# Kernel tuning notes

Hardware: AMD Instinct MI355X
Metric: run time of the kernel (lower is better)

The kernel has to match this reference:

```python
import jax, jax.numpy as jnp
import numpy as np

COMMITMENT_COST = 0.25
EMBEDDING_COST = 1.0


def setup_inputs() -> dict:
    key = jax.random.key(0)
    k1, k2 = jax.random.split(key)
    x = jax.random.normal(k1, (64, 1024, 64), dtype=jnp.float32)
    embeddings = jax.random.normal(k2, (1024, 64), dtype=jnp.float32)
    return {"x": x, "embeddings": embeddings}


def reference(x, embeddings):
    D = embeddings.shape[1]
    flat_x = x.reshape(-1, D)  # [N, D]
    distances = (
        jnp.sum(flat_x ** 2, axis=1, keepdims=True)
        + jnp.sum(embeddings ** 2, axis=1)
        - 2.0 * flat_x @ embeddings.T
    )
    encoding_indices = jnp.argmin(distances, axis=1)  # [N]
    quantized = embeddings[encoding_indices].reshape(x.shape)
    q_latent_loss = jnp.mean((quantized - jax.lax.stop_gradient(x)) ** 2) * EMBEDDING_COST
    e_latent_loss = jnp.mean((x - jax.lax.stop_gradient(quantized)) ** 2) * COMMITMENT_COST
    loss = q_latent_loss + e_latent_loss
    # Straight-through estimator
    quantized_st = x + jax.lax.stop_gradient(quantized - x)
    return (quantized_st, loss)
```

## Files before the change

kernel.cpp:

```cpp
#include <hip/hip_runtime.h>
#include <math.h>

#define NROWS 65536
#define D 64
#define K 1024
#define BR 64
#define EC 128
#define NCH (K / EC)
#define THREADS 256
#define TAU 0.02f
#define LOSS_SCALE (1.25f / (65536.0f * 64.0f))

typedef short bf16x8 __attribute__((ext_vector_type(8)));
typedef float f32x4 __attribute__((ext_vector_type(4)));

__device__ inline unsigned short f2bf(float f) {
    unsigned int u = __float_as_uint(f);
    unsigned int r = u + 0x7fffu + ((u >> 16) & 1u);
    return (unsigned short)(r >> 16);
}
__device__ inline float bf2f(unsigned short h) {
    return __uint_as_float(((unsigned int)h) << 16);
}
__device__ inline void cvt8(const float4& a, const float4& b, bf16x8& h, bf16x8& l) {
    float f[8] = {a.x, a.y, a.z, a.w, b.x, b.y, b.z, b.w};
#pragma unroll
    for (int j = 0; j < 8; ++j) {
        unsigned short hb = f2bf(f[j]);
        h[j] = (short)hb;
        l[j] = (short)f2bf(f[j] - bf2f(hb));
    }
}

__global__ void vq_prep(const float* __restrict__ E, float* __restrict__ C,
                        bf16x8* __restrict__ Eh8, bf16x8* __restrict__ El8,
                        float* __restrict__ lossp, int* __restrict__ fcnt) {
    int k = blockIdx.x * blockDim.x + threadIdx.x;
    if (k == 0) { *lossp = 0.f; *fcnt = 0; }
    if (k >= K) return;
    const float4* ev = (const float4*)(E + (size_t)k * D);
    float s = 0.f;
#pragma unroll
    for (int u = 0; u < 8; ++u) {
        float4 a = ev[2 * u], b = ev[2 * u + 1];
        s = fmaf(a.x, a.x, s); s = fmaf(a.y, a.y, s);
        s = fmaf(a.z, a.z, s); s = fmaf(a.w, a.w, s);
        s = fmaf(b.x, b.x, s); s = fmaf(b.y, b.y, s);
        s = fmaf(b.z, b.z, s); s = fmaf(b.w, b.w, s);
        bf16x8 h, l;
        cvt8(a, b, h, l);
        Eh8[(size_t)k * 8 + u] = h;
        El8[(size_t)k * 8 + u] = l;
    }
    C[k] = s;
}

__global__ __launch_bounds__(THREADS, 4) void vq_main(
    const float* __restrict__ X, const float* __restrict__ E,
    const float* __restrict__ C,
    const bf16x8* __restrict__ Eh8, const bf16x8* __restrict__ El8,
    int* __restrict__ bestk, int* __restrict__ flags, int* __restrict__ fcnt,
    float* __restrict__ out, float* __restrict__ lossp)
{
    __shared__ bf16x8 sEh8[EC * 8];
    __shared__ bf16x8 sEl8[EC * 8];
    __shared__ float  sCn[EC];
    __shared__ int    sIdx[BR];
    __shared__ float  sLoss[4];

    const int t    = threadIdx.x;
    const int w    = t >> 6;
    const int lane = t & 63;
    const int l15  = lane & 15;
    const int l4   = lane >> 4;

    const float4* Xg4 = (const float4*)X;

    size_t abase = ((size_t)blockIdx.x * BR + w * 16 + l15) * 16;
    bf16x8 ah[2], al[2];
    float nrm = 0.f;
#pragma unroll
    for (int kt = 0; kt < 2; ++kt) {
        float4 fa = Xg4[abase + kt * 8 + l4 * 2];
        float4 fb = Xg4[abase + kt * 8 + l4 * 2 + 1];
        nrm = fmaf(fa.x, fa.x, nrm); nrm = fmaf(fa.y, fa.y, nrm);
        nrm = fmaf(fa.z, fa.z, nrm); nrm = fmaf(fa.w, fa.w, nrm);
        nrm = fmaf(fb.x, fb.x, nrm); nrm = fmaf(fb.y, fb.y, nrm);
        nrm = fmaf(fb.z, fb.z, nrm); nrm = fmaf(fb.w, fb.w, nrm);
        cvt8(fa, fb, ah[kt], al[kt]);
    }
    nrm += __shfl_xor(nrm, 16, 64);
    nrm += __shfl_xor(nrm, 32, 64);
    float rxv[4];
#pragma unroll
    for (int r = 0; r < 4; ++r) rxv[r] = __shfl(nrm, l4 * 4 + r, 64);

    float m[4], m2[4]; int bk[4];
#pragma unroll
    for (int r = 0; r < 4; ++r) { m[r] = INFINITY; m2[r] = INFINITY; bk[r] = 0; }

    for (int ch = 0; ch < NCH; ++ch) {
        __syncthreads();
#pragma unroll
        for (int p = 0; p < 4; ++p) {
            int S = p * 256 + t;
            int code = S >> 3, u8 = S & 7;
            int di = code * 8 + (u8 ^ (code & 7));
            sEh8[di] = Eh8[(size_t)ch * (EC * 8) + S];
            sEl8[di] = El8[(size_t)ch * (EC * 8) + S];
        }
        if (t < EC) sCn[t] = C[ch * EC + t];
        __syncthreads();

#pragma unroll 2
        for (int pr = 0; pr < 4; ++pr) {
            int c0 = pr * 32 + l15;
            int c1 = c0 + 16;
            int s0 = c0 & 7, s1 = c1 & 7;
            bf16x8 bh00 = sEh8[c0 * 8 + (l4 ^ s0)];
            bf16x8 bh01 = sEh8[c0 * 8 + ((4 + l4) ^ s0)];
            bf16x8 bl00 = sEl8[c0 * 8 + (l4 ^ s0)];
            bf16x8 bl01 = sEl8[c0 * 8 + ((4 + l4) ^ s0)];
            bf16x8 bh10 = sEh8[c1 * 8 + (l4 ^ s1)];
            bf16x8 bh11 = sEh8[c1 * 8 + ((4 + l4) ^ s1)];
            bf16x8 bl10 = sEl8[c1 * 8 + (l4 ^ s1)];
            bf16x8 bl11 = sEl8[c1 * 8 + ((4 + l4) ^ s1)];

            f32x4 h0 = {0.f, 0.f, 0.f, 0.f}, x0 = {0.f, 0.f, 0.f, 0.f};
            f32x4 h1 = {0.f, 0.f, 0.f, 0.f}, x1 = {0.f, 0.f, 0.f, 0.f};
            h0 = __builtin_amdgcn_mfma_f32_16x16x32_bf16(ah[0], bh00, h0, 0, 0, 0);
            h1 = __builtin_amdgcn_mfma_f32_16x16x32_bf16(ah[0], bh10, h1, 0, 0, 0);
            x0 = __builtin_amdgcn_mfma_f32_16x16x32_bf16(al[0], bh00, x0, 0, 0, 0);
            x1 = __builtin_amdgcn_mfma_f32_16x16x32_bf16(al[0], bh10, x1, 0, 0, 0);
            h0 = __builtin_amdgcn_mfma_f32_16x16x32_bf16(ah[1], bh01, h0, 0, 0, 0);
            h1 = __builtin_amdgcn_mfma_f32_16x16x32_bf16(ah[1], bh11, h1, 0, 0, 0);
            x0 = __builtin_amdgcn_mfma_f32_16x16x32_bf16(ah[0], bl00, x0, 0, 0, 0);
            x1 = __builtin_amdgcn_mfma_f32_16x16x32_bf16(ah[0], bl10, x1, 0, 0, 0);
            x0 = __builtin_amdgcn_mfma_f32_16x16x32_bf16(al[1], bh01, x0, 0, 0, 0);
            x1 = __builtin_amdgcn_mfma_f32_16x16x32_bf16(al[1], bh11, x1, 0, 0, 0);
            x0 = __builtin_amdgcn_mfma_f32_16x16x32_bf16(ah[1], bl01, x0, 0, 0, 0);
            x1 = __builtin_amdgcn_mfma_f32_16x16x32_bf16(ah[1], bl11, x1, 0, 0, 0);

            float ce0 = sCn[pr * 32 + l15];
            float ce1 = sCn[pr * 32 + 16 + l15];
            int k0 = ch * EC + pr * 32 + l15;
            int k1 = k0 + 16;
#pragma unroll
            for (int r = 0; r < 4; ++r) {
                float d0 = fmaf(-2.f, h0[r] + x0[r], rxv[r] + ce0);
                m2[r] = fminf(m2[r], fmaxf(m[r], d0));
                bk[r] = (d0 < m[r]) ? k0 : bk[r];
                m[r]  = fminf(m[r], d0);
                float d1 = fmaf(-2.f, h1[r] + x1[r], rxv[r] + ce1);
                m2[r] = fminf(m2[r], fmaxf(m[r], d1));
                bk[r] = (d1 < m[r]) ? k1 : bk[r];
                m[r]  = fminf(m[r], d1);
            }
        }
    }

#pragma unroll
    for (int r = 0; r < 4; ++r) {
        float mm = m[r], mm2 = m2[r]; int kk = bk[r];
#pragma unroll
        for (int off = 1; off < 16; off <<= 1) {
            float om  = __shfl_xor(mm,  off, 64);
            float om2 = __shfl_xor(mm2, off, 64);
            int   ok  = __shfl_xor(kk,  off, 64);
            mm2 = fminf(fminf(mm2, om2), fmaxf(mm, om));
            if (om < mm || (om == mm && ok < kk)) { mm = om; kk = ok; }
        }
        if (l15 == 0) {
            int lr = w * 16 + l4 * 4 + r;
            sIdx[lr] = kk;
            if (mm2 - mm < TAU) {
                int pos = atomicAdd(fcnt, 1);
                flags[pos] = blockIdx.x * BR + lr;
            }
        }
    }
    __syncthreads();

    {
        int row = t >> 2, q = t & 3;
        int kb = sIdx[row];
        size_t grow = (size_t)blockIdx.x * BR + row;
        if (q == 0) bestk[grow] = kb;
        const float4* eq   = (const float4*)E + (size_t)kb * 16;
        const float4* xrow = Xg4 + grow * 16;
        float4* orow = (float4*)out + grow * 16;
        float ls = 0.f;
#pragma unroll
        for (int j = 0; j < 4; ++j) {
            int u = q * 4 + j;
            float4 qv = eq[u];
            float4 xv = xrow[u];
            orow[u] = qv;
            float dx = qv.x - xv.x; ls = fmaf(dx, dx, ls);
            float dy = qv.y - xv.y; ls = fmaf(dy, dy, ls);
            float dz = qv.z - xv.z; ls = fmaf(dz, dz, ls);
            float dw = qv.w - xv.w; ls = fmaf(dw, dw, ls);
        }
#pragma unroll
        for (int off = 32; off > 0; off >>= 1) ls += __shfl_down(ls, off, 64);
        if (lane == 0) sLoss[w] = ls;
        __syncthreads();
        if (t == 0)
            atomicAdd(lossp, (sLoss[0] + sLoss[1] + sLoss[2] + sLoss[3]) * LOSS_SCALE);
    }
}

__global__ __launch_bounds__(64) void vq_fix(
    const float* __restrict__ X, const float* __restrict__ E,
    const float* __restrict__ C,
    const int* __restrict__ bestk, const int* __restrict__ flags,
    const int* __restrict__ fcnt,
    float* __restrict__ out, float* __restrict__ lossp)
{
    __shared__ float4 sx4[16];
    const int lane = threadIdx.x;
    const float4* Eg4 = (const float4*)E;
    int nf = *fcnt;

    for (int i = blockIdx.x; i < nf; i += gridDim.x) {
        int row = flags[i];
        float xd = X[(size_t)row * D + lane];
        ((float*)sx4)[lane] = xd;
        float rx = xd * xd;
#pragma unroll
        for (int off = 1; off < 64; off <<= 1) rx += __shfl_xor(rx, off, 64);
        __syncthreads();

        float mm = INFINITY; int kb = 0;
        for (int jj = 0; jj < K / 64; ++jj) {
            int kk = jj * 64 + lane;
            const float4* er = Eg4 + (size_t)kk * 16;
            float a0 = 0.f, a1 = 0.f, a2 = 0.f, a3 = 0.f;
#pragma unroll
            for (int p = 0; p < 16; p += 4) {
                float4 xv0 = sx4[p],     e0 = er[p];
                float4 xv1 = sx4[p + 1], e1 = er[p + 1];
                float4 xv2 = sx4[p + 2], e2 = er[p + 2];
                float4 xv3 = sx4[p + 3], e3 = er[p + 3];
                a0 = fmaf(xv0.x, e0.x, a0); a0 = fmaf(xv0.y, e0.y, a0);
                a0 = fmaf(xv0.z, e0.z, a0); a0 = fmaf(xv0.w, e0.w, a0);
                a1 = fmaf(xv1.x, e1.x, a1); a1 = fmaf(xv1.y, e1.y, a1);
                a1 = fmaf(xv1.z, e1.z, a1); a1 = fmaf(xv1.w, e1.w, a1);
                a2 = fmaf(xv2.x, e2.x, a2); a2 = fmaf(xv2.y, e2.y, a2);
                a2 = fmaf(xv2.z, e2.z, a2); a2 = fmaf(xv2.w, e2.w, a2);
                a3 = fmaf(xv3.x, e3.x, a3); a3 = fmaf(xv3.y, e3.y, a3);
                a3 = fmaf(xv3.z, e3.z, a3); a3 = fmaf(xv3.w, e3.w, a3);
            }
            float dot = (a0 + a1) + (a2 + a3);
            float dd = fmaf(-2.f, dot, rx + C[kk]);
            if (dd < mm) { mm = dd; kb = kk; }
        }
#pragma unroll
        for (int off = 1; off < 64; off <<= 1) {
            float om = __shfl_xor(mm, off, 64);
            int   ok = __shfl_xor(kb, off, 64);
            if (om < mm || (om == mm && ok < kb)) { mm = om; kb = ok; }
        }
        int ko = bestk[row];
        if (kb != ko) {
            if (lane < 16) {
                float4 qn = Eg4[(size_t)kb * 16 + lane];
                float4 qo = Eg4[(size_t)ko * 16 + lane];
                float4 xv = sx4[lane];
                float dl = 0.f;
                float a, b2;
                a = qn.x - xv.x; b2 = qo.x - xv.x; dl += a * a - b2 * b2;
                a = qn.y - xv.y; b2 = qo.y - xv.y; dl += a * a - b2 * b2;
                a = qn.z - xv.z; b2 = qo.z - xv.z; dl += a * a - b2 * b2;
                a = qn.w - xv.w; b2 = qo.w - xv.w; dl += a * a - b2 * b2;
#pragma unroll
                for (int off = 1; off < 16; off <<= 1) dl += __shfl_xor(dl, off, 16);
                ((float4*)out)[(size_t)row * 16 + lane] = qn;
                if (lane == 0) atomicAdd(lossp, dl * LOSS_SCALE);
            }
        }
        __syncthreads();
    }
}

extern "C" void kernel_launch(void* const* d_in, const int* in_sizes, int n_in,
                              void* d_out, int out_size, void* d_ws, size_t ws_size,
                              hipStream_t stream) {
    const float* X = (const float*)d_in[0];
    const float* E = (const float*)d_in[1];
    float* out   = (float*)d_out;
    float* lossp = out + (size_t)NROWS * D;

    float* C     = (float*)d_ws;
    int*   bestk = (int*)d_ws + 1024;
    int*   flags = (int*)d_ws + 1024 + 65536;
    int*   fcnt  = (int*)d_ws + 1024 + 2 * 65536;
    bf16x8* Eh8  = (bf16x8*)((int*)d_ws + 1024 + 2 * 65536 + 4);
    bf16x8* El8  = Eh8 + (size_t)K * 8;

    vq_prep<<<(K + 255) / 256, 256, 0, stream>>>(E, C, Eh8, El8, lossp, fcnt);

    vq_main<<<NROWS / BR, THREADS, 0, stream>>>(
        X, E, C, Eh8, El8, bestk, flags, fcnt, out, lossp);

    vq_fix<<<1024, 64, 0, stream>>>(X, E, C, bestk, flags, fcnt, out, lossp);
}
```

Measured before the change: 72.26 us.

## Double-tile rows per wave, prefetch codebook chunks, and maximize half-norm-shifted dot

Each wave now handles 32 rows (two 16-row tiles) with BR=128, so each codebook fragment read from shared memory feeds twice as many MFMAs. The next codebook chunk is prefetched into registers while the current one is computed, which overlaps global loads with MFMA work. The distance is rewritten as maximizing x·e − ||e||²/2, which drops the ||x||² term and the multiply by −2. The ambiguity threshold is rescaled to match, and launch bounds drop to two blocks per CU, trading occupancy for more registers.

Result: no change. 71.55 us (-1.0%).

```diff
diff --git a/kernel.cpp b/kernel.cpp
--- a/kernel.cpp
+++ b/kernel.cpp
@@ -4,11 +4,11 @@
 #define NROWS 65536
 #define D 64
 #define K 1024
-#define BR 64
+#define BR 128
 #define EC 128
 #define NCH (K / EC)
 #define THREADS 256
-#define TAU 0.02f
+#define TAU_S 0.005f
 #define LOSS_SCALE (1.25f / (65536.0f * 64.0f))
 
 typedef short bf16x8 __attribute__((ext_vector_type(8)));
@@ -33,6 +33,7 @@
 }
 
 __global__ void vq_prep(const float* __restrict__ E, float* __restrict__ C,
+                        float* __restrict__ Ch,
                         bf16x8* __restrict__ Eh8, bf16x8* __restrict__ El8,
                         float* __restrict__ lossp, int* __restrict__ fcnt) {
     int k = blockIdx.x * blockDim.x + threadIdx.x;
@@ -53,11 +54,12 @@
         El8[(size_t)k * 8 + u] = l;
     }
     C[k] = s;
-}
-
-__global__ __launch_bounds__(THREADS, 4) void vq_main(
+    Ch[k] = 0.5f * s;
+}
+
+__global__ __launch_bounds__(THREADS, 2) void vq_main(
     const float* __restrict__ X, const float* __restrict__ E,
-    const float* __restrict__ C,
+    const float* __restrict__ Ch,
     const bf16x8* __restrict__ Eh8, const bf16x8* __restrict__ El8,
     int* __restrict__ bestk, int* __restrict__ flags, int* __restrict__ fcnt,
     float* __restrict__ out, float* __restrict__ lossp)
@@ -76,123 +78,135 @@
 
     const float4* Xg4 = (const float4*)X;
 
-    size_t abase = ((size_t)blockIdx.x * BR + w * 16 + l15) * 16;
-    bf16x8 ah[2], al[2];
-    float nrm = 0.f;
-#pragma unroll
-    for (int kt = 0; kt < 2; ++kt) {
-        float4 fa = Xg4[abase + kt * 8 + l4 * 2];
-        float4 fb = Xg4[abase + kt * 8 + l4 * 2 + 1];
-        nrm = fmaf(fa.x, fa.x, nrm); nrm = fmaf(fa.y, fa.y, nrm);
-        nrm = fmaf(fa.z, fa.z, nrm); nrm = fmaf(fa.w, fa.w, nrm);
-        nrm = fmaf(fb.x, fb.x, nrm); nrm = fmaf(fb.y, fb.y, nrm);
-        nrm = fmaf(fb.z, fb.z, nrm); nrm = fmaf(fb.w, fb.w, nrm);
-        cvt8(fa, fb, ah[kt], al[kt]);
-    }
-    nrm += __shfl_xor(nrm, 16, 64);
-    nrm += __shfl_xor(nrm, 32, 64);
-    float rxv[4];
-#pragma unroll
-    for (int r = 0; r < 4; ++r) rxv[r] = __shfl(nrm, l4 * 4 + r, 64);
-
-    float m[4], m2[4]; int bk[4];
-#pragma unroll
-    for (int r = 0; r < 4; ++r) { m[r] = INFINITY; m2[r] = INFINITY; bk[r] = 0; }
+    bf16x8 ah[2][2], al[2][2];
+#pragma unroll
+    for (int rt = 0; rt < 2; ++rt) {
+        size_t abase = ((size_t)blockIdx.x * BR + w * 32 + rt * 16 + l15) * 16;
+#pragma unroll
+        for (int kt = 0; kt < 2; ++kt) {
+            float4 fa = Xg4[abase + kt * 8 + l4 * 2];
+            float4 fb = Xg4[abase + kt * 8 + l4 * 2 + 1];
+            cvt8(fa, fb, ah[rt][kt], al[rt][kt]);
+        }
+    }
+
+    float m[2][4], m2[2][4]; int bk[2][4];
+#pragma unroll
+    for (int rt = 0; rt < 2; ++rt)
+#pragma unroll
+        for (int r = 0; r < 4; ++r) { m[rt][r] = -INFINITY; m2[rt][r] = -INFINITY; bk[rt][r] = 0; }
+
+    bf16x8 rh[4], rl[4];
+    float creg = 0.f;
+#pragma unroll
+    for (int p = 0; p < 4; ++p) {
+        int S = p * 256 + t;
+        rh[p] = Eh8[S];
+        rl[p] = El8[S];
+    }
+    if (t < EC) creg = Ch[t];
+#pragma unroll
+    for (int p = 0; p < 4; ++p) {
+        int S = p * 256 + t;
+        int code = S >> 3, u8 = S & 7;
+        int di = code * 8 + (u8 ^ (code & 7));
+        sEh8[di] = rh[p];
+        sEl8[di] = rl[p];
+    }
+    if (t < EC) sCn[t] = creg;
+    __syncthreads();
 
     for (int ch = 0; ch < NCH; ++ch) {
-        __syncthreads();
-#pragma unroll
-        for (int p = 0; p < 4; ++p) {
-            int S = p * 256 + t;
-            int code = S >> 3, u8 = S & 7;
-            int di = code * 8 + (u8 ^ (code & 7));
-            sEh8[di] = Eh8[(size_t)ch * (EC * 8) + S];
-            sEl8[di] = El8[(size_t)ch * (EC * 8) + S];
-        }
-        if (t < EC) sCn[t] = C[ch * EC + t];
-        __syncthreads();
+        if (ch + 1 < NCH) {
+#pragma unroll
+            for (int p = 0; p < 4; ++p) {
+                int S = p * 256 + t;
+                rh[p] = Eh8[(size_t)(ch + 1) * (EC * 8) + S];
+                rl[p] = El8[(size_t)(ch + 1) * (EC * 8) + S];
+            }
+            if (t < EC) creg = Ch[(ch + 1) * EC + t];
+        }
 
 #pragma unroll 2
-        for (int pr = 0; pr < 4; ++pr) {
-            int c0 = pr * 32 + l15;
-            int c1 = c0 + 16;
-            int s0 = c0 & 7, s1 = c1 & 7;
-            bf16x8 bh00 = sEh8[c0 * 8 + (l4 ^ s0)];
-            bf16x8 bh01 = sEh8[c0 * 8 + ((4 + l4) ^ s0)];
-            bf16x8 bl00 = sEl8[c0 * 8 + (l4 ^ s0)];
-            bf16x8 bl01 = sEl8[c0 * 8 + ((4 + l4) ^ s0)];
-            bf16x8 bh10 = sEh8[c1 * 8 + (l4 ^ s1)];
-            bf16x8 bh11 = sEh8[c1 * 8 + ((4 + l4) ^ s1)];
-            bf16x8 bl10 = sEl8[c1 * 8 + (l4 ^ s1)];
-            bf16x8 bl11 = sEl8[c1 * 8 + ((4 + l4) ^ s1)];
-
-            f32x4 h0 = {0.f, 0.f, 0.f, 0.f}, x0 = {0.f, 0.f, 0.f, 0.f};
-            f32x4 h1 = {0.f, 0.f, 0.f, 0.f}, x1 = {0.f, 0.f, 0.f, 0.f};
-            h0 = __builtin_amdgcn_mfma_f32_16x16x32_bf16(ah[0], bh00, h0, 0, 0, 0);
-            h1 = __builtin_amdgcn_mfma_f32_16x16x32_bf16(ah[0], bh10, h1, 0, 0, 0);
-            x0 = __builtin_amdgcn_mfma_f32_16x16x32_bf16(al[0], bh00, x0, 0, 0, 0);
-            x1 = __builtin_amdgcn_mfma_f32_16x16x32_bf16(al[0], bh10, x1, 0, 0, 0);
-            h0 = __builtin_amdgcn_mfma_f32_16x16x32_bf16(ah[1], bh01, h0, 0, 0, 0);
-            h1 = __builtin_amdgcn_mfma_f32_16x16x32_bf16(ah[1], bh11, h1, 0, 0, 0);
-            x0 = __builtin_amdgcn_mfma_f32_16x16x32_bf16(ah[0], bl00, x0, 0, 0, 0);
-            x1 = __builtin_amdgcn_mfma_f32_16x16x32_bf16(ah[0], bl10, x1, 0, 0, 0);
-            x0 = __builtin_amdgcn_mfma_f32_16x16x32_bf16(al[1], bh01, x0, 0, 0, 0);
-            x1 = __builtin_amdgcn_mfma_f32_16x16x32_bf16(al[1], bh11, x1, 0, 0, 0);
-            x0 = __builtin_amdgcn_mfma_f32_16x16x32_bf16(ah[1], bl01, x0, 0, 0, 0);
-            x1 = __builtin_amdgcn_mfma_f32_16x16x32_bf16(ah[1], bl11, x1, 0, 0, 0);
-
-            float ce0 = sCn[pr * 32 + l15];
-            float ce1 = sCn[pr * 32 + 16 + l15];
-            int k0 = ch * EC + pr * 32 + l15;
-            int k1 = k0 + 16;
-#pragma unroll
-            for (int r = 0; r < 4; ++r) {
-                float d0 = fmaf(-2.f, h0[r] + x0[r], rxv[r] + ce0);
-                m2[r] = fminf(m2[r], fmaxf(m[r], d0));
-                bk[r] = (d0 < m[r]) ? k0 : bk[r];
-                m[r]  = fminf(m[r], d0);
-                float d1 = fmaf(-2.f, h1[r] + x1[r], rxv[r] + ce1);
-                m2[r] = fminf(m2[r], fmaxf(m[r], d1));
-                bk[r] = (d1 < m[r]) ? k1 : bk[r];
-                m[r]  = fminf(m[r], d1);
-            }
-        }
-    }
-
-#pragma unroll
-    for (int r = 0; r < 4; ++r) {
-        float mm = m[r], mm2 = m2[r]; int kk = bk[r];
-#pragma unroll
-        for (int off = 1; off < 16; off <<= 1) {
-            float om  = __shfl_xor(mm,  off, 64);
-            float om2 = __shfl_xor(mm2, off, 64);
-            int   ok  = __shfl_xor(kk,  off, 64);
-            mm2 = fminf(fminf(mm2, om2), fmaxf(mm, om));
-            if (om < mm || (om == mm && ok < kk)) { mm = om; kk = ok; }
-        }
-        if (l15 == 0) {
-            int lr = w * 16 + l4 * 4 + r;
-            sIdx[lr] = kk;
-            if (mm2 - mm < TAU) {
-                int pos = atomicAdd(fcnt, 1);
-                flags[pos] = blockIdx.x * BR + lr;
-            }
-        }
-    }
+        for (int t8 = 0; t8 < 8; ++t8) {
+            int code = t8 * 16 + l15;
+            int cs = code & 7;
+            bf16x8 bh0 = sEh8[code * 8 + (l4 ^ cs)];
+            bf16x8 bh1 = sEh8[code * 8 + ((4 + l4) ^ cs)];
+            bf16x8 bl0 = sEl8[code * 8 + (l4 ^ cs)];
+            bf16x8 bl1 = sEl8[code * 8 + ((4 + l4) ^ cs)];
+            float ce2 = sCn[code];
+            int kk = ch * EC + code;
+
+#pragma unroll
+            for (int rt = 0; rt < 2; ++rt) {
+                f32x4 h = {0.f, 0.f, 0.f, 0.f}, x = {0.f, 0.f, 0.f, 0.f};
+                h = __builtin_amdgcn_mfma_f32_16x16x32_bf16(ah[rt][0], bh0, h, 0, 0, 0);
+                x = __builtin_amdgcn_mfma_f32_16x16x32_bf16(al[rt][0], bh0, x, 0, 0, 0);
+                h = __builtin_amdgcn_mfma_f32_16x16x32_bf16(ah[rt][1], bh1, h, 0, 0, 0);
+                x = __builtin_amdgcn_mfma_f32_16x16x32_bf16(al[rt][1], bh1, x, 0, 0, 0);
+                x = __builtin_amdgcn_mfma_f32_16x16x32_bf16(ah[rt][0], bl0, x, 0, 0, 0);
+                x = __builtin_amdgcn_mfma_f32_16x16x32_bf16(ah[rt][1], bl1, x, 0, 0, 0);
+#pragma unroll
+                for (int r = 0; r < 4; ++r) {
+                    float v = (h[r] + x[r]) - ce2;
+                    m2[rt][r] = fmaxf(m2[rt][r], fminf(m[rt][r], v));
+                    bk[rt][r] = (v > m[rt][r]) ? kk : bk[rt][r];
+                    m[rt][r]  = fmaxf(m[rt][r], v);
+                }
+            }
+        }
+        __syncthreads();
+        if (ch + 1 < NCH) {
+#pragma unroll
+            for (int p = 0; p < 4; ++p) {
+                int S = p * 256 + t;
+                int code = S >> 3, u8 = S & 7;
+                int di = code * 8 + (u8 ^ (code & 7));
+                sEh8[di] = rh[p];
+                sEl8[di] = rl[p];
+            }
+            if (t < EC) sCn[t] = creg;
+        }
+        __syncthreads();
+    }
+
+#pragma unroll
+    for (int rt = 0; rt < 2; ++rt)
+#pragma unroll
+        for (int r = 0; r < 4; ++r) {
+            float mm = m[rt][r], mm2 = m2[rt][r]; int kk = bk[rt][r];
+#pragma unroll
+            for (int off = 1; off < 16; off <<= 1) {
+                float om  = __shfl_xor(mm,  off, 64);
+                float om2 = __shfl_xor(mm2, off, 64);
+                int   ok  = __shfl_xor(kk,  off, 64);
+                mm2 = fmaxf(fmaxf(mm2, om2), fminf(mm, om));
+                if (om > mm || (om == mm && ok < kk)) { mm = om; kk = ok; }
+            }
+            if (l15 == 0) {
+                int lr = w * 32 + rt * 16 + l4 * 4 + r;
+                sIdx[lr] = kk;
+                if (mm - mm2 < TAU_S) {
+                    int pos = atomicAdd(fcnt, 1);
+                    flags[pos] = blockIdx.x * BR + lr;
+                }
+            }
+        }
     __syncthreads();
 
     {
-        int row = t >> 2, q = t & 3;
+        int row = t >> 1, half = t & 1;
         int kb = sIdx[row];
         size_t grow = (size_t)blockIdx.x * BR + row;
-        if (q == 0) bestk[grow] = kb;
+        if (half == 0) bestk[grow] = kb;
         const float4* eq   = (const float4*)E + (size_t)kb * 16;
         const float4* xrow = Xg4 + grow * 16;
         float4* orow = (float4*)out + grow * 16;
         float ls = 0.f;
 #pragma unroll
-        for (int j = 0; j < 4; ++j) {
-            int u = q * 4 + j;
+        for (int j = 0; j < 8; ++j) {
+            int u = half * 8 + j;
             float4 qv = eq[u];
             float4 xv = xrow[u];
             orow[u] = qv;
@@ -292,16 +306,17 @@
     float* lossp = out + (size_t)NROWS * D;
 
     float* C     = (float*)d_ws;
-    int*   bestk = (int*)d_ws + 1024;
-    int*   flags = (int*)d_ws + 1024 + 65536;
-    int*   fcnt  = (int*)d_ws + 1024 + 2 * 65536;
-    bf16x8* Eh8  = (bf16x8*)((int*)d_ws + 1024 + 2 * 65536 + 4);
+    float* Ch    = (float*)d_ws + 1024;
+    int*   bestk = (int*)d_ws + 2048;
+    int*   flags = (int*)d_ws + 2048 + 65536;
+    int*   fcnt  = (int*)d_ws + 2048 + 2 * 65536;
+    bf16x8* Eh8  = (bf16x8*)((int*)d_ws + 2048 + 2 * 65536 + 4);
     bf16x8* El8  = Eh8 + (size_t)K * 8;
 
-    vq_prep<<<(K + 255) / 256, 256, 0, stream>>>(E, C, Eh8, El8, lossp, fcnt);
+    vq_prep<<<(K + 255) / 256, 256, 0, stream>>>(E, C, Ch, Eh8, El8, lossp, fcnt);
 
     vq_main<<<NROWS / BR, THREADS, 0, stream>>>(
-        X, E, C, Eh8, El8, bestk, flags, fcnt, out, lossp);
-
-    vq_fix<<<1024, 64, 0, stream>>>(X, E, C, bestk, flags, fcnt, out, lossp);
-}
+        X, E, Ch, Eh8, El8, bestk, flags, fcnt, out, lossp);
+
+    vq_fix<<<512, 64, 0, stream>>>(X, E, C, bestk, flags, fcnt, out, lossp);
+}
```
